# Performance work log

Hardware: AMD Instinct MI355X
Metric: run time of the kernel (lower is better)

The kernel has to match this reference:

```python
import jax, jax.numpy as jnp
import numpy as np

EPS = 1e-5  # equinox LayerNorm default eps

def setup_inputs() -> dict:
    key = jax.random.key(0)
    k1, k2, k3, k4, k5 = jax.random.split(key, 5)
    heads, d, dH, N = 16, 1024, 64, 2048
    # lecun-normal-ish scaling for fan_in=d
    s = 1.0 / np.sqrt(d)
    return {
        "x": jax.random.normal(k1, (d, N), dtype=jnp.float32),
        "WQ": jax.random.normal(k2, (heads, d, dH), dtype=jnp.float32) * s,
        "WK": jax.random.normal(k3, (heads, d, dH), dtype=jnp.float32) * s,
        "WV": jax.random.normal(k4, (heads, d, dH), dtype=jnp.float32) * s,
        "W0": jax.random.normal(k5, (d, d), dtype=jnp.float32) * s,
    }

def reference(x, WQ, WK, WV, W0):
    # x: [d, N]
    residual = x
    # equinox LayerNorm over full shape (d, N), no affine params
    mean = jnp.mean(x)
    var = jnp.var(x)
    xn = (x - mean) * jax.lax.rsqrt(var + EPS)
    # project: [h, d_model, dH] x [d_model, N] -> [h, dH, N]
    Q = jnp.einsum('hcd,ci->hdi', WQ, xn)
    K = jnp.einsum('hcd,ci->hdi', WK, xn)
    V = jnp.einsum('hcd,ci->hdi', WV, xn)
    dH = WK.shape[-1]
    dot = jnp.einsum('hdi,hdj->hij', Q, K)  # [h, N, N]
    alpha = jax.nn.softmax(dot / jnp.sqrt(jnp.asarray(dH, dot.dtype)), axis=-1)
    attn = jnp.einsum('hij,hdj->hdi', alpha, V)  # [h, dH, N]
    N = attn.shape[2]
    attn = attn.reshape(-1, N)  # [d, N]
    out = W0 @ attn
    return out + residual
```

## Files before the change

### kernel.cpp

```cpp
#include <hip/hip_runtime.h>
#include <math.h>

typedef unsigned short u16;
typedef _Float16 f16;
typedef __attribute__((ext_vector_type(8))) short bf16x8;
typedef __attribute__((ext_vector_type(4))) float f32x4;
typedef __attribute__((ext_vector_type(4))) f16 f16x4;

#define D_MODEL 1024
#define SEQ_N   2048
#define HEADS   16
#define DHEAD   64
#define M3      3072
#define JSPLIT  2
#define JCHUNK  (SEQ_N / JSPLIT)
#define NIT     (JCHUNK / 64)
#define QSCALE  0.18033688011112042f
#define EXPOFF  5.770780163555854f

#define GLOBAL_AS __attribute__((address_space(1)))
#define LDS_AS    __attribute__((address_space(3)))
#define ASYNC16(gp, lp) __builtin_amdgcn_global_load_lds( \
    (const GLOBAL_AS unsigned int*)(gp), (LDS_AS unsigned int*)(lp), 16, 0, 0)

__device__ __forceinline__ u16 f2bf(float f) {
  union { float f; unsigned int u; } v; v.f = f;
  unsigned int r = v.u + 0x7fffu + ((v.u >> 16) & 1u);
  return (u16)(r >> 16);
}

__global__ __launch_bounds__(256) void prep(const float* __restrict__ x,
                                            double* __restrict__ part,
                                            const float* __restrict__ WQ,
                                            const float* __restrict__ WK,
                                            const float* __restrict__ WV,
                                            const float* __restrict__ W0,
                                            u16* __restrict__ Wp,
                                            u16* __restrict__ W0p) {
  __shared__ double ls[256], lss[256];
  __shared__ float tile[32][65];
  int t = threadIdx.x;
  int b = blockIdx.x;
  if (b < 256) {
    const float4* x4 = (const float4*)x;
    const int n4 = (D_MODEL * SEQ_N) / 4;
    double s = 0.0, ss = 0.0;
    for (int idx = b * 256 + t; idx < n4; idx += 256 * 256) {
      float4 v = x4[idx];
      s  += (double)v.x + (double)v.y + (double)v.z + (double)v.w;
      ss += (double)v.x * v.x + (double)v.y * v.y + (double)v.z * v.z + (double)v.w * v.w;
    }
    ls[t] = s; lss[t] = ss;
    __syncthreads();
    for (int off = 128; off > 0; off >>= 1) {
      if (t < off) { ls[t] += ls[t + off]; lss[t] += lss[t + off]; }
      __syncthreads();
    }
    if (t == 0) { part[2 * b] = ls[0]; part[2 * b + 1] = lss[0]; }
    return;
  }
  int f = b - 256;
  int z = f >> 9;
  int rem = f & 511;
  if (z == 3) {
    int idx = rem * 512 + t;
#pragma unroll
    for (int r = 0; r < 2; ++r, idx += 256) {
      float4 v = ((const float4*)W0)[idx];
      unsigned int lo = (unsigned int)f2bf(v.x) | ((unsigned int)f2bf(v.y) << 16);
      unsigned int hi = (unsigned int)f2bf(v.z) | ((unsigned int)f2bf(v.w) << 16);
      uint2 o; o.x = lo; o.y = hi;
      *(uint2*)(&W0p[(size_t)idx * 4]) = o;
    }
    return;
  }
  const float* W = (z == 0) ? WQ : ((z == 1) ? WK : WV);
  int h = rem >> 5, cb = (rem & 31) * 32;
  int dh = t & 63, cl = t >> 6;
  for (int r = 0; r < 8; ++r) {
    int c = cl + r * 4;
    tile[c][dh] = W[((size_t)h * D_MODEL + cb + c) * DHEAD + dh];
  }
  __syncthreads();
  int c2 = t & 31, d2 = t >> 5;
  for (int r = 0; r < 8; ++r) {
    int dd = d2 + r * 8;
    Wp[(size_t)((z * HEADS + h) * DHEAD + dd) * D_MODEL + cb + c2] = f2bf(tile[c2][dd]);
  }
}

__global__ __launch_bounds__(256) void ln_norm_t(const float* __restrict__ x,
                                                 const double* __restrict__ part,
                                                 u16* __restrict__ xnt) {
  __shared__ double ls[256], lss[256];
  __shared__ float tile[64][65];
  int t = threadIdx.x;
  ls[t] = part[2 * t]; lss[t] = part[2 * t + 1];
  __syncthreads();
  for (int off = 128; off > 0; off >>= 1) {
    if (t < off) { ls[t] += ls[t + off]; lss[t] += lss[t + off]; }
    __syncthreads();
  }
  double inv = 1.0 / ((double)D_MODEL * (double)SEQ_N);
  double m = ls[0] * inv;
  double vv = lss[0] * inv - m * m;
  float mean = (float)m;
  float rstd = (float)(1.0 / sqrt(vv + 1e-5));

  int ib = blockIdx.x * 64, cb = blockIdx.y * 64;
  int il = t & 63, cl = t >> 6;
  for (int r = 0; r < 16; ++r) {
    int c = cl + r * 4;
    tile[c][il] = (x[(size_t)(cb + c) * SEQ_N + ib + il] - mean) * rstd;
  }
  __syncthreads();
  int c2 = t & 63, i2 = t >> 6;
  for (int r = 0; r < 16; ++r) {
    int i = i2 + r * 4;
    xnt[(size_t)(ib + i) * D_MODEL + cb + c2] = f2bf(tile[c2][i]);
  }
}

__global__ __launch_bounds__(256) void gemm_qkv(const u16* __restrict__ A,
                                                const u16* __restrict__ Bt,
                                                u16* __restrict__ Qt,
                                                u16* __restrict__ Kt,
                                                f16* __restrict__ Vb) {
  __shared__ __align__(16) u16 Alds[2 * 2 * 96 * 32];
  __shared__ __align__(16) u16 Blds[2 * 2 * 128 * 32];
  int t = threadIdx.x;
  int lane = t & 63, w = t >> 6;
  int g = lane >> 4, l16 = lane & 15;
  int wr = w >> 1, wc = w & 1;
  int flat = blockIdx.x;
  int wi = flat >> 3;
  int wx = wi & 7, wy = wi >> 3;
  int cx = (flat & 7) & 1, cy = (flat & 7) >> 1;
  int bx = cx * 8 + wx;
  int by = cy * 8 + wy;
  int mb = by * 96, nb = bx * 128;

  f32x4 acc[3][4];
#pragma unroll
  for (int i = 0; i < 3; ++i)
#pragma unroll
    for (int j = 0; j < 4; ++j) acc[i][j] = (f32x4){0.f, 0.f, 0.f, 0.f};

  const u16* AgP[3]; int ldsA[3];
#pragma unroll
  for (int r = 0; r < 3; ++r) {
    int idx = r * 256 + t;
    int kk = (idx >= 384) ? 1 : 0;
    int rem = idx - kk * 384;
    int row = rem >> 2, c4 = rem & 3;
    int csw = c4 ^ ((row >> 1) & 3);
    AgP[r] = A + (size_t)(mb + row) * D_MODEL + kk * 32 + csw * 8;
    ldsA[r] = idx * 8;
  }
  const u16* BgP[4]; int ldsB[4];
#pragma unroll
  for (int r = 0; r < 4; ++r) {
    int idx = r * 256 + t;
    int kk = idx >> 9;
    int rem = idx & 511;
    int row = rem >> 2, c4 = rem & 3;
    int csw = c4 ^ ((row >> 1) & 3);
    BgP[r] = Bt + (size_t)(nb + row) * D_MODEL + kk * 32 + csw * 8;
    ldsB[r] = idx * 8;
  }

#pragma unroll
  for (int r = 0; r < 3; ++r) ASYNC16(AgP[r], &Alds[ldsA[r]]);
#pragma unroll
  for (int r = 0; r < 4; ++r) ASYNC16(BgP[r], &Blds[ldsB[r]]);
#pragma unroll
  for (int r = 0; r < 3; ++r) ASYNC16(AgP[r] + 64, &Alds[6144 + ldsA[r]]);
#pragma unroll
  for (int r = 0; r < 4; ++r) ASYNC16(BgP[r] + 64, &Blds[8192 + ldsB[r]]);

  int rowa0 = wr * 48, rowb0 = wc * 64;
  int cur = 0;
  for (int ks = 0; ks < 16; ++ks) {
    if (ks < 15) asm volatile("s_waitcnt vmcnt(7)" ::: "memory");
    else         asm volatile("s_waitcnt vmcnt(0)" ::: "memory");
    __builtin_amdgcn_s_barrier();
#pragma unroll
    for (int kk = 0; kk < 2; ++kk) {
      bf16x8 af[3], bf[4];
#pragma unroll
      for (int tm = 0; tm < 3; ++tm) {
        int row = rowa0 + tm * 16 + l16;
        int gs = g ^ ((row >> 1) & 3);
        af[tm] = *(const bf16x8*)(&Alds[cur * 6144 + kk * 3072 + row * 32 + gs * 8]);
      }
#pragma unroll
      for (int tn = 0; tn < 4; ++tn) {
        int row = rowb0 + tn * 16 + l16;
        int gs = g ^ ((row >> 1) & 3);
        bf[tn] = *(const bf16x8*)(&Blds[cur * 8192 + kk * 4096 + row * 32 + gs * 8]);
      }
#pragma unroll
      for (int tm = 0; tm < 3; ++tm)
#pragma unroll
        for (int tn = 0; tn < 4; ++tn)
          acc[tm][tn] = __builtin_amdgcn_mfma_f32_16x16x32_bf16(af[tm], bf[tn],
                                                                acc[tm][tn], 0, 0, 0);
    }
    __builtin_amdgcn_s_barrier();
    if (ks + 2 < 16) {
      int kb = (ks + 2) * 64;
#pragma unroll
      for (int r = 0; r < 3; ++r) ASYNC16(AgP[r] + kb, &Alds[cur * 6144 + ldsA[r]]);
#pragma unroll
      for (int r = 0; r < 4; ++r) ASYNC16(BgP[r] + kb, &Blds[cur * 8192 + ldsB[r]]);
    }
    cur ^= 1;
  }

#pragma unroll
  for (int tm = 0; tm < 3; ++tm) {
    int row0 = mb + wr * 48 + tm * 16 + g * 4;
#pragma unroll
    for (int tn = 0; tn < 4; ++tn) {
      int col = nb + wc * 64 + tn * 16 + l16;
      if (row0 < 2 * D_MODEL) {
        u16* T = (row0 < D_MODEL) ? Qt : Kt;
        float sc = (row0 < D_MODEL) ? QSCALE : 1.0f;
        int rbase = (row0 < D_MODEL) ? row0 : row0 - D_MODEL;
        ushort4 o;
        o.x = f2bf(acc[tm][tn][0] * sc); o.y = f2bf(acc[tm][tn][1] * sc);
        o.z = f2bf(acc[tm][tn][2] * sc); o.w = f2bf(acc[tm][tn][3] * sc);
        *(ushort4*)(&T[(size_t)col * D_MODEL + rbase]) = o;
      } else {
        int rbase = row0 - 2 * D_MODEL;
#pragma unroll
        for (int r = 0; r < 4; ++r)
          Vb[(size_t)(rbase + r) * SEQ_N + col] = (f16)acc[tm][tn][r];
      }
    }
  }
}

__global__ __launch_bounds__(256) void gemm_bf16(const u16* __restrict__ A,
                                                 const u16* __restrict__ Bt,
                                                 float* __restrict__ C,
                                                 const float* __restrict__ res,
                                                 int M, int N, int K) {
  __shared__ __align__(16) u16 Alds[2 * 2 * 64 * 32];
  __shared__ __align__(16) u16 Blds[2 * 2 * 64 * 32];
  int t = threadIdx.x;
  int w = t >> 6, lane = t & 63;
  int g = lane >> 4, l16 = lane & 15;
  int flat = blockIdx.x;
  int wi = flat >> 3;
  int wx = wi & 7, wy = wi >> 3;
  int cx = (flat & 7) & 3, cy = (flat & 7) >> 2;
  int bx = cx * 8 + wx;
  int by = cy * 8 + wy;
  int mb = by * 64, nb = bx * 64;
  f32x4 acc[4];
  for (int i = 0; i < 4; ++i) acc[i] = (f32x4){0.f, 0.f, 0.f, 0.f};

  const u16* AgP[2]; const u16* BgP[2]; int ldsO[2];
#pragma unroll
  for (int r = 0; r < 2; ++r) {
    int idx = r * 256 + t;
    int kk = idx >> 8;
    int rem = idx & 255;
    int row = rem >> 2, c4 = rem & 3;
    int csw = c4 ^ ((row >> 1) & 3);
    AgP[r] = A + (size_t)(mb + row) * K + kk * 32 + csw * 8;
    BgP[r] = Bt + (size_t)(nb + row) * K + kk * 32 + csw * 8;
    ldsO[r] = idx * 8;
  }

#pragma unroll
  for (int r = 0; r < 2; ++r) { ASYNC16(AgP[r], &Alds[ldsO[r]]); ASYNC16(BgP[r], &Blds[ldsO[r]]); }
#pragma unroll
  for (int r = 0; r < 2; ++r) {
    ASYNC16(AgP[r] + 64, &Alds[4096 + ldsO[r]]);
    ASYNC16(BgP[r] + 64, &Blds[4096 + ldsO[r]]);
  }

  int cur = 0;
  const int NK = 16;
  for (int ks = 0; ks < NK; ++ks) {
    if (ks < NK - 1) asm volatile("s_waitcnt vmcnt(4)" ::: "memory");
    else             asm volatile("s_waitcnt vmcnt(0)" ::: "memory");
    __builtin_amdgcn_s_barrier();
#pragma unroll
    for (int kk = 0; kk < 2; ++kk) {
      int rowa = w * 16 + l16;
      int gsa = g ^ ((rowa >> 1) & 3);
      bf16x8 af = *(const bf16x8*)(&Alds[cur * 4096 + kk * 2048 + rowa * 32 + gsa * 8]);
#pragma unroll
      for (int tn = 0; tn < 4; ++tn) {
        int rowb = tn * 16 + l16;
        int gsb = g ^ ((rowb >> 1) & 3);
        bf16x8 bf = *(const bf16x8*)(&Blds[cur * 4096 + kk * 2048 + rowb * 32 + gsb * 8]);
        acc[tn] = __builtin_amdgcn_mfma_f32_16x16x32_bf16(af, bf, acc[tn], 0, 0, 0);
      }
    }
    __builtin_amdgcn_s_barrier();
    if (ks + 2 < NK) {
      int kb = (ks + 2) * 64;
#pragma unroll
      for (int r = 0; r < 2; ++r) {
        ASYNC16(AgP[r] + kb, &Alds[cur * 4096 + ldsO[r]]);
        ASYNC16(BgP[r] + kb, &Blds[cur * 4096 + ldsO[r]]);
      }
    }
    cur ^= 1;
  }
  int col0 = nb + l16;
  int row0 = mb + w * 16 + g * 4;
#pragma unroll
  for (int tn = 0; tn < 4; ++tn) {
    int col = col0 + tn * 16;
#pragma unroll
    for (int r = 0; r < 4; ++r) {
      int row = row0 + r;
      float v = acc[tn][r];
      if (res) v += res[(size_t)row * N + col];
      C[(size_t)row * N + col] = v;
    }
  }
}

#define KSW(buf_, row_, ch_) ((buf_)*4096 + (row_)*64 + ((((ch_) ^ ((row_)&7)))*8))
__global__ __launch_bounds__(256, 2) void attn_mfma(const u16* __restrict__ Qt,
                                                    const u16* __restrict__ Kt,
                                                    const f16* __restrict__ Vb,
                                                    f16* __restrict__ Opart,
                                                    float* __restrict__ Lpart) {
  __shared__ __align__(16) u16 Klds[2 * 64 * 64];
  __shared__ __align__(16) f16 Vlds[2 * 64 * 64];
  int flat = blockIdx.x;
  int xcd = flat & 7, idx = flat >> 3;
  int h  = xcd * 2 + ((idx >> 5) & 1);
  int sp = idx >> 6;
  int ib = (idx & 31) * 64;
  int j0 = sp * JCHUNK;
  int t = threadIdx.x;
  int w = t >> 6, lane = t & 63;
  int g = lane >> 4, l16 = lane & 15;

  bf16x8 bq[2];
  {
    const u16* qb = Qt + (size_t)(ib + w * 16 + l16) * D_MODEL + h * DHEAD + g * 8;
    bq[0] = *(const bf16x8*)(qb);
    bq[1] = *(const bf16x8*)(qb + 32);
  }

  f32x4 acc_o[4];
#pragma unroll
  for (int i = 0; i < 4; ++i) acc_o[i] = (f32x4){0.f, 0.f, 0.f, 0.f};
  f32x4 acc_l = (f32x4){0.f, 0.f, 0.f, 0.f};
  f16x4 ones;
  ones[0] = (f16)1.f; ones[1] = (f16)1.f; ones[2] = (f16)1.f; ones[3] = (f16)1.f;

  int srow = t >> 2, sc0 = (t & 3) * 16;
  int c0 = (t & 3) * 2;
  const u16* Kg = Kt + (size_t)(j0 + srow) * D_MODEL + h * DHEAD + sc0;
  const f16* Vg = Vb + (size_t)(h * DHEAD + srow) * SEQ_N + j0 + sc0;

  uint4 ka = *(const uint4*)(Kg);
  uint4 kb = *(const uint4*)(Kg + 8);
  uint4 va = *(const uint4*)(Vg);
  uint4 vb = *(const uint4*)(Vg + 8);
  *(uint4*)(&Klds[KSW(0, srow, c0)])     = ka;
  *(uint4*)(&Klds[KSW(0, srow, c0 + 1)]) = kb;
  *(uint4*)(&Vlds[KSW(0, srow, c0)])     = va;
  *(uint4*)(&Vlds[KSW(0, srow, c0 + 1)]) = vb;
  __syncthreads();

  int cur = 0;
  for (int it = 0; it < NIT; ++it) {
    if (it + 1 < NIT) {
      const u16* Kn = Kg + (size_t)(it + 1) * 64 * D_MODEL;
      const f16* Vn = Vg + (it + 1) * 64;
      ka = *(const uint4*)(Kn);
      kb = *(const uint4*)(Kn + 8);
      va = *(const uint4*)(Vn);
      vb = *(const uint4*)(Vn + 8);
    }

    f32x4 s[4];
#pragma unroll
    for (int i = 0; i < 4; ++i) s[i] = (f32x4){0.f, 0.f, 0.f, 0.f};
    __builtin_amdgcn_s_setprio(1);
#pragma unroll
    for (int kk = 0; kk < 2; ++kk)
#pragma unroll
      for (int tn = 0; tn < 4; ++tn) {
        int row = tn * 16 + l16;
        bf16x8 ak = *(const bf16x8*)(&Klds[KSW(cur, row, kk * 4 + g)]);
        s[tn] = __builtin_amdgcn_mfma_f32_16x16x32_bf16(ak, bq[kk], s[tn], 0, 0, 0);
      }
    __builtin_amdgcn_s_setprio(0);
    f16x4 pf[4];
#pragma unroll
    for (int tn = 0; tn < 4; ++tn) {
      f16x4 p;
#pragma unroll
      for (int r = 0; r < 4; ++r)
        p[r] = (f16)exp2f(s[tn][r] - EXPOFF);
      pf[tn] = p;
    }
    __builtin_amdgcn_s_setprio(1);
#pragma unroll
    for (int tn = 0; tn < 4; ++tn) {
      acc_l = __builtin_amdgcn_mfma_f32_16x16x16f16(pf[tn], ones, acc_l, 0, 0, 0);
#pragma unroll
      for (int td = 0; td < 4; ++td) {
        int row = td * 16 + l16;
        f16x4 bv = *(const f16x4*)(&Vlds[KSW(cur, row, tn * 2 + (g >> 1)) + (g & 1) * 4]);
        acc_o[td] =
            __builtin_amdgcn_mfma_f32_16x16x16f16(pf[tn], bv, acc_o[td], 0, 0, 0);
      }
    }
    __builtin_amdgcn_s_setprio(0);

    if (it + 1 < NIT) {
      *(uint4*)(&Klds[KSW(cur ^ 1, srow, c0)])     = ka;
      *(uint4*)(&Klds[KSW(cur ^ 1, srow, c0 + 1)]) = kb;
      *(uint4*)(&Vlds[KSW(cur ^ 1, srow, c0)])     = va;
      *(uint4*)(&Vlds[KSW(cur ^ 1, srow, c0 + 1)]) = vb;
    }
    __syncthreads();
    cur ^= 1;
  }

  if (l16 == 0) {
#pragma unroll
    for (int r = 0; r < 4; ++r)
      Lpart[((size_t)sp * HEADS + h) * SEQ_N + ib + w * 16 + g * 4 + r] = acc_l[r];
  }

#pragma unroll
  for (int td = 0; td < 4; ++td) {
    int dh = h * DHEAD + td * 16 + l16;
#pragma unroll
    for (int r = 0; r < 4; ++r) {
      int i = ib + w * 16 + g * 4 + r;
      Opart[((size_t)sp * SEQ_N + i) * D_MODEL + dh] = (f16)acc_o[td][r];
    }
  }
}

__global__ __launch_bounds__(256) void attn_combine(const f16* __restrict__ Opart,
                                                    const float* __restrict__ Lpart,
                                                    u16* __restrict__ attnt) {
  int i = blockIdx.x;
  int c = threadIdx.x * 4;
  int h = c >> 6;
  float l = 0.f;
#pragma unroll
  for (int s = 0; s < JSPLIT; ++s) l += Lpart[((size_t)s * HEADS + h) * SEQ_N + i];
  float o[4] = {0.f, 0.f, 0.f, 0.f};
#pragma unroll
  for (int s = 0; s < JSPLIT; ++s) {
    f16x4 v = *(const f16x4*)(&Opart[((size_t)s * SEQ_N + i) * D_MODEL + c]);
#pragma unroll
    for (int r = 0; r < 4; ++r) o[r] += (float)v[r];
  }
  float inv = 1.0f / l;
  ushort4 ob;
  ob.x = f2bf(o[0] * inv); ob.y = f2bf(o[1] * inv);
  ob.z = f2bf(o[2] * inv); ob.w = f2bf(o[3] * inv);
  *(ushort4*)(&attnt[(size_t)i * D_MODEL + c]) = ob;
}

extern "C" void kernel_launch(void* const* d_in, const int* in_sizes, int n_in,
                              void* d_out, int out_size, void* d_ws, size_t ws_size,
                              hipStream_t stream) {
  const float* x  = (const float*)d_in[0];
  const float* WQ = (const float*)d_in[1];
  const float* WK = (const float*)d_in[2];
  const float* WV = (const float*)d_in[3];
  const float* W0 = (const float*)d_in[4];
  float* out = (float*)d_out;

  char* ws = (char*)d_ws;
  size_t off = 0;
  double* part  = (double*)(ws + off); off += 8192;
  u16*    xnt   = (u16*)(ws + off); off += (size_t)SEQ_N * D_MODEL * 2;
  u16*    Wp    = (u16*)(ws + off); off += (size_t)M3 * D_MODEL * 2;
  u16*    W0p   = (u16*)(ws + off); off += (size_t)D_MODEL * D_MODEL * 2;
  u16*    Qt    = (u16*)(ws + off); off += (size_t)SEQ_N * D_MODEL * 2;
  u16*    Kt    = (u16*)(ws + off); off += (size_t)SEQ_N * D_MODEL * 2;
  f16*    Vb    = (f16*)(ws + off); off += (size_t)D_MODEL * SEQ_N * 2;
  u16*    attnt = (u16*)(ws + off); off += (size_t)SEQ_N * D_MODEL * 2;
  f16*    Opart = (f16*)(ws + off); off += (size_t)JSPLIT * SEQ_N * D_MODEL * 2;
  float*  Lpart = (float*)(ws + off); off += (size_t)JSPLIT * HEADS * SEQ_N * 4;

  prep<<<256 + 2048, 256, 0, stream>>>(x, part, WQ, WK, WV, W0, Wp, W0p);
  ln_norm_t<<<dim3(SEQ_N / 64, D_MODEL / 64), 256, 0, stream>>>(x, part, xnt);
  gemm_qkv<<<512, 256, 0, stream>>>(Wp, xnt, Qt, Kt, Vb);
  attn_mfma<<<1024, 256, 0, stream>>>(Qt, Kt, Vb, Opart, Lpart);
  attn_combine<<<SEQ_N, 256, 0, stream>>>(Opart, Lpart, attnt);
  gemm_bf16<<<512, 256, 0, stream>>>(W0p, attnt, out, x, D_MODEL, SEQ_N, D_MODEL);
}
```

Baseline: 153.7 us.

## Stream K/V tiles into LDS with async global_load_lds double buffering

Replaces the register-staged K/V prefetch (global load into registers, then store to LDS) in the attention loop with direct global-to-LDS async loads, issued two tiles ahead. Waits use explicit vmcnt counts and raw s_barrier instead of __syncthreads. The goal is to cut VGPR pressure and LDS write instructions and overlap memory with MFMA work. It relies on the async write pattern matching the KSW swizzle layout and on the vmcnt accounting being correct, so a mismatch would corrupt the results.

New measurement: 151.5 us (median of 2 runs). About the same (-1.5%).

```diff
diff --git a/kernel.cpp b/kernel.cpp
--- a/kernel.cpp
+++ b/kernel.cpp
@@ -359,31 +359,30 @@
   f16x4 ones;
   ones[0] = (f16)1.f; ones[1] = (f16)1.f; ones[2] = (f16)1.f; ones[3] = (f16)1.f;
 
-  int srow = t >> 2, sc0 = (t & 3) * 16;
-  int c0 = (t & 3) * 2;
-  const u16* Kg = Kt + (size_t)(j0 + srow) * D_MODEL + h * DHEAD + sc0;
-  const f16* Vg = Vb + (size_t)(h * DHEAD + srow) * SEQ_N + j0 + sc0;
-
-  uint4 ka = *(const uint4*)(Kg);
-  uint4 kb = *(const uint4*)(Kg + 8);
-  uint4 va = *(const uint4*)(Vg);
-  uint4 vb = *(const uint4*)(Vg + 8);
-  *(uint4*)(&Klds[KSW(0, srow, c0)])     = ka;
-  *(uint4*)(&Klds[KSW(0, srow, c0 + 1)]) = kb;
-  *(uint4*)(&Vlds[KSW(0, srow, c0)])     = va;
-  *(uint4*)(&Vlds[KSW(0, srow, c0 + 1)]) = vb;
-  __syncthreads();
+  const u16* KgP[2]; const f16* VgP[2]; int ldsS[2];
+#pragma unroll
+  for (int r = 0; r < 2; ++r) {
+    int s = r * 256 + t;
+    int row = s >> 3, pch = s & 7;
+    int lch = pch ^ (row & 7);
+    KgP[r] = Kt + (size_t)(j0 + row) * D_MODEL + h * DHEAD + lch * 8;
+    VgP[r] = Vb + (size_t)(h * DHEAD + row) * SEQ_N + j0 + lch * 8;
+    ldsS[r] = s * 8;
+  }
+
+#pragma unroll
+  for (int r = 0; r < 2; ++r) { ASYNC16(KgP[r], &Klds[ldsS[r]]); ASYNC16(VgP[r], &Vlds[ldsS[r]]); }
+#pragma unroll
+  for (int r = 0; r < 2; ++r) {
+    ASYNC16(KgP[r] + 64 * D_MODEL, &Klds[4096 + ldsS[r]]);
+    ASYNC16(VgP[r] + 64,           &Vlds[4096 + ldsS[r]]);
+  }
 
   int cur = 0;
   for (int it = 0; it < NIT; ++it) {
-    if (it + 1 < NIT) {
-      const u16* Kn = Kg + (size_t)(it + 1) * 64 * D_MODEL;
-      const f16* Vn = Vg + (it + 1) * 64;
-      ka = *(const uint4*)(Kn);
-      kb = *(const uint4*)(Kn + 8);
-      va = *(const uint4*)(Vn);
-      vb = *(const uint4*)(Vn + 8);
-    }
+    if (it < NIT - 1) asm volatile("s_waitcnt vmcnt(4)" ::: "memory");
+    else              asm volatile("s_waitcnt vmcnt(0)" ::: "memory");
+    __builtin_amdgcn_s_barrier();
 
     f32x4 s[4];
 #pragma unroll
@@ -421,13 +420,15 @@
     }
     __builtin_amdgcn_s_setprio(0);
 
-    if (it + 1 < NIT) {
-      *(uint4*)(&Klds[KSW(cur ^ 1, srow, c0)])     = ka;
-      *(uint4*)(&Klds[KSW(cur ^ 1, srow, c0 + 1)]) = kb;
-      *(uint4*)(&Vlds[KSW(cur ^ 1, srow, c0)])     = va;
-      *(uint4*)(&Vlds[KSW(cur ^ 1, srow, c0 + 1)]) = vb;
-    }
-    __syncthreads();
+    __builtin_amdgcn_s_barrier();
+    if (it + 2 < NIT) {
+      int joff = (it + 2) * 64;
+#pragma unroll
+      for (int r = 0; r < 2; ++r) {
+        ASYNC16(KgP[r] + (size_t)joff * D_MODEL, &Klds[cur * 4096 + ldsS[r]]);
+        ASYNC16(VgP[r] + joff,                   &Vlds[cur * 4096 + ldsS[r]]);
+      }
+    }
     cur ^= 1;
   }
 
```
